# Kernel optimization log

Measured on AMD Instinct MI355X. Metric: run time of the kernel, lower is better.

Reference implementation:

```python
import jax, jax.numpy as jnp
import numpy as np

K = 9            # connections per output pixel
GA = 2           # global additional samples
RA = 2           # relative additional samples
VS = 4 + GA + RA # 2^rank neighbours + sampled
REGION = 12      # int(0.25 * 48) per spatial dim
MMULT = 0.1
MIN_SIGMA = 0.05
SIGMA_SCALE = 0.05
SIGMA_BOOST = 2.0


def setup_inputs() -> dict:
    key = jax.random.key(0)
    ks = jax.random.split(key, 8)
    b, cin, h, w = 8, 128, 48, 48
    cout = 256
    hidden = cin * 4

    def lin_init(k, fan_out, fan_in):
        bound = 1.0 / np.sqrt(fan_in)
        kw, kb = jax.random.split(k)
        W = jax.random.uniform(kw, (fan_out, fan_in), minval=-bound, maxval=bound, dtype=jnp.float32)
        bb = jax.random.uniform(kb, (fan_out,), minval=-bound, maxval=bound, dtype=jnp.float32)
        return W, bb

    x = jax.random.normal(ks[0], (b, cin, h, w), dtype=jnp.float32)
    W1, b1 = lin_init(ks[1], hidden, 2)          # toparams layer 1 (adaptive=False -> 2 coord inputs)
    W2, b2 = lin_init(ks[2], 3 * K, hidden)      # toparams layer 2 -> k means (2d) + k sigmas
    Wu, bu = lin_init(ks[3], cout, K * cin)      # unify linear
    gints = jax.random.randint(ks[4], (b, h, w, K, GA, 2), 0, h, dtype=jnp.int32)      # global samples (h==w)
    roff = jax.random.randint(ks[5], (b, h, w, K, RA, 2), 0, REGION, dtype=jnp.int32)  # relative offsets
    return {"x": x, "W1": W1, "b1": b1, "W2": W2, "b2": b2, "Wu": Wu, "bu": bu,
            "gints": gints, "roff": roff}


def reference(x, W1, b1, W2, b2, Wu, bu, gints, roff):
    b, c, h, w = x.shape
    s = jnp.array([h, w], dtype=x.dtype)                       # spatial range per dim
    s_int = jnp.array([h, w], dtype=jnp.int32)

    # normalized coordinate grid in [0,1], (h, w, 2) with [.,.,0]=row, [.,.,1]=col
    rows = jnp.arange(h, dtype=x.dtype) / (h - 1)
    cols = jnp.arange(w, dtype=x.dtype) / (w - 1)
    coords = jnp.stack(jnp.meshgrid(rows, cols, indexing='ij'), axis=-1)

    # hypernetwork: per-pixel coords -> K 2d mean offsets + K sigmas
    inp = jnp.broadcast_to(coords, (b, h, w, 2))
    hid = jax.nn.relu(inp @ W1.T + b1)
    params = hid @ W2.T + b2                                   # (b,h,w,3K)
    means_raw = params[..., :2 * K].reshape(b, h, w, K, 2)
    sig_raw = params[..., 2 * K:]                              # (b,h,w,K)

    # mids: inverse of the sigmoid scaling applied to the pixel's own coordinate
    pix = coords * (s - 1)                                     # pixel coordinates
    sc = pix / (s - 1) * 0.9999 + 0.00005
    mids = jnp.log(sc / (1.0 - sc))                            # (h,w,2)

    # transform_means: sigmoid -> [0, s-1]
    means = jax.nn.sigmoid(mids[None, :, :, None, :] + MMULT * means_raw) * (s - 1)  # (b,h,w,K,2)
    # transform_sigmas: softplus(. + boost) + min, per-dim scale, then sigma_scale
    sigmas = (jax.nn.softplus(sig_raw + SIGMA_BOOST) + MIN_SIGMA)[..., None] * s * SIGMA_SCALE  # (b,h,w,K,2)

    # ---- integer index generation (non-differentiable) ----
    fl = jnp.floor(jax.lax.stop_gradient(means)).astype(jnp.int32)   # (b,h,w,K,2)
    combos = jnp.array([[0, 0], [0, 1], [1, 0], [1, 1]], dtype=jnp.int32)
    neigh = fl[..., None, :] + combos                                 # (b,h,w,K,4,2)
    rel = fl[..., None, :] + roff - REGION // 2                       # (b,h,w,K,RA,2)
    ints = jnp.concatenate([neigh, gints, rel], axis=-2) % s_int      # (b,h,w,K,VS,2)

    # duplicate masking: zero any tuple that occurred earlier along VS
    eq = jnp.all(ints[..., :, None, :] == ints[..., None, :, :], axis=-1)  # (...,VS,VS)
    lower = jnp.tril(jnp.ones((VS, VS), dtype=bool), k=-1)
    dups = jnp.any(eq & lower, axis=-1)                               # (b,h,w,K,VS)

    # unnormalized gaussian densities of integer points under (means, sigmas)
    diff = (ints.astype(x.dtype) - means[..., None, :]) / sigmas[..., None, :]
    props = jnp.exp(-0.5 * jnp.sum(diff * diff, axis=-1))             # (b,h,w,K,VS)
    props = jnp.where(dups, jnp.zeros((), x.dtype), props)
    weights = props / jnp.sum(props, axis=-1, keepdims=True)          # mvalues are all-ones

    # irregular gather of input channel vectors at sampled pixels
    lin = ints[..., 0] * w + ints[..., 1]                             # (b,h,w,K,VS)
    flat = x.transpose(0, 2, 3, 1).reshape(b, h * w, c)
    feats = flat[jnp.arange(b)[:, None], lin.reshape(b, -1)]          # (b, h*w*K*VS, c)
    feats = feats.reshape(b, h, w, K, VS, c)

    feats = jnp.einsum('bhwkvc,bhwkv->bhwkc', feats, weights)         # weighted reduce over VS
    feats = feats.reshape(b, h, w, K * c)
    out = feats @ Wu.T + bu                                           # unify linear
    return out.transpose(0, 3, 1, 2)                                  # (b, cout, h, w)
```

## Files before the change

kernel.cpp:

```cpp
#include <hip/hip_runtime.h>
#include <hip/hip_bf16.h>
#include <hip/hip_fp16.h>

#define BB 8
#define CIN 128
#define HH 48
#define WW 48
#define HW 2304
#define KK 9
#define COUT 256
#define KC 1152
#define MM 18432
#define MT 32
#define SFP 136
#define NP 5

#define LIGHT_BARRIER() asm volatile("s_waitcnt lgkmcnt(0)\n\ts_barrier" ::: "memory")

typedef short bf16x8_t __attribute__((ext_vector_type(8)));
typedef float f32x16_t __attribute__((ext_vector_type(16)));
typedef float f32x4_t  __attribute__((ext_vector_type(4)));

static __device__ __forceinline__ float b2f(short u) {
    union { unsigned int i; float f; } c;
    c.i = ((unsigned int)(unsigned short)u) << 16;
    return c.f;
}

__global__ __launch_bounds__(256) void prep_kernel(
    const float* __restrict__ x, __hip_bfloat16* __restrict__ xT,
    const float* __restrict__ Wu, bf16x8_t* __restrict__ Bp,
    const float* __restrict__ W1, const float* __restrict__ b1,
    const float* __restrict__ W2, const float* __restrict__ b2,
    float* __restrict__ means, float* __restrict__ sigmas, int* __restrict__ fls)
{
    int bid = blockIdx.x;
    int t = threadIdx.x;

    if (bid < 576) {
        __shared__ float tile[64][65];
        int ij0 = (bid % 36) * 64;
        int c0  = ((bid / 36) % 2) * 64;
        int b   = bid / 72;
        int ijl = t & 63, cl = t >> 6;
        #pragma unroll
        for (int i = 0; i < 16; i++) {
            int cc = i*4 + cl;
            tile[cc][ijl] = x[(size_t)(b*CIN + c0 + cc) * HW + ij0 + ijl];
        }
        __syncthreads();
        int cl2 = t & 63, ijl2 = t >> 6;
        #pragma unroll
        for (int i = 0; i < 16; i++) {
            int ij = i*4 + ijl2;
            xT[(size_t)(b*HW + ij0 + ij) * CIN + c0 + cl2] = __float2bfloat16(tile[cl2][ij]);
        }
    } else if (bid < 720) {
        int idx = (bid - 576) * 256 + t;
        int lane = idx & 63;
        int rest = idx >> 6;
        int s = rest % 72, g = rest / 72;
        int r = lane & 31, qq = lane >> 5;
        const float* src = Wu + (size_t)(g*32 + r) * KC + s*16 + qq*8;
        union { bf16x8_t v; __hip_bfloat16 h[8]; } o;
        #pragma unroll
        for (int j = 0; j < 8; j++) o.h[j] = __float2bfloat16(src[j]);
        Bp[idx] = o.v;
    } else {
        int wave = t >> 6, lane = t & 63;
        int p = (bid - 720) * 4 + wave;
        int iy = p / WW, ix = p % WW;
        float ryf = (float)iy / 47.0f;
        float rxf = (float)ix / 47.0f;
        double ry = (double)ryf, rx = (double)rxf;

        double h[8];
        #pragma unroll
        for (int jj = 0; jj < 8; jj++) {
            int j = lane*8 + jj;
            double v = ry * (double)W1[j*2+0] + rx * (double)W1[j*2+1] + (double)b1[j];
            h[jj] = v > 0.0 ? v : 0.0;
        }
        double par[27];
        #pragma unroll
        for (int o = 0; o < 27; o++) {
            const float4* w4 = (const float4*)(W2 + (size_t)o*512 + lane*8);
            float4 wa = w4[0], wb = w4[1];
            double s = (double)wa.x*h[0] + (double)wa.y*h[1]
                     + (double)wa.z*h[2] + (double)wa.w*h[3]
                     + (double)wb.x*h[4] + (double)wb.y*h[5]
                     + (double)wb.z*h[6] + (double)wb.w*h[7];
            par[o] = s;
        }
        #pragma unroll
        for (int o = 0; o < 27; o++) {
            #pragma unroll
            for (int d = 1; d < 64; d <<= 1)
                par[o] += __shfl_xor(par[o], d, 64);
            par[o] += (double)b2[o];
        }
        if (lane < KK) {
            int k = lane;
            double scy = ry * 0.9999 + 5e-05;
            double scx = rx * 0.9999 + 5e-05;
            double midy = log(scy / (1.0 - scy));
            double midx = log(scx / (1.0 - scx));
            double zy = midy + 0.1 * par[2*k+0];
            double zx = midx + 0.1 * par[2*k+1];
            double my = 47.0 / (1.0 + exp(-zy));
            double mx = 47.0 / (1.0 + exp(-zx));
            double sr = par[18 + k] + 2.0;
            double sp = (sr > 0.0 ? sr : 0.0) + log1p(exp(-fabs(sr)));
            double sg = (sp + 0.05) * 48.0 * 0.05;
            means[(p*KK + k)*2 + 0] = (float)my;
            means[(p*KK + k)*2 + 1] = (float)mx;
            sigmas[p*KK + k] = (float)sg;
            fls[(p*KK + k)*2 + 0] = (int)floor(my);
            fls[(p*KK + k)*2 + 1] = (int)floor(mx);
        }
    }
}

__global__ __launch_bounds__(512, 4) void fused_kernel(
    const float* __restrict__ means, const float* __restrict__ sigmas,
    const int* __restrict__ fls, const int* __restrict__ gints,
    const int* __restrict__ roff, const short* __restrict__ xT,
    const bf16x8_t* __restrict__ Bp, const float* __restrict__ bu,
    float* __restrict__ out)
{
    __shared__ unsigned int s_tap[KK*MT*8];
    __shared__ __align__(16) short s_feat[2][2][MT*SFP];

    int t = threadIdx.x;
    int b   = blockIdx.x & 7;
    int grp = blockIdx.x >> 3;
    int ij0 = grp * MT;
    int m0  = b * HW + ij0;

    if (t < KK*MT) {
        int p = t;
        int k = p >> 5, row = p & 31;
        int ij = ij0 + row;
        int bij = m0 + row;
        int fy = fls[(ij*KK + k)*2 + 0];
        int fx = fls[(ij*KK + k)*2 + 1];
        float my = means[(ij*KK + k)*2 + 0];
        float mx = means[(ij*KK + k)*2 + 1];
        float sg = sigmas[ij*KK + k];
        int lins[8]; float ws[8];
        #pragma unroll
        for (int v = 0; v < 8; v++) {
            int iy, ix;
            if (v < 4) {
                iy = fy + (v >> 1); ix = fx + (v & 1);
            } else if (v < 6) {
                int base = ((bij*KK + k)*2 + (v - 4)) * 2;
                iy = gints[base]; ix = gints[base + 1];
            } else {
                int base = ((bij*KK + k)*2 + (v - 6)) * 2;
                iy = fy + roff[base] - 6; ix = fx + roff[base + 1] - 6;
            }
            iy = ((iy % HH) + HH) % HH;
            ix = ((ix % WW) + WW) % WW;
            lins[v] = iy * WW + ix;
            float dy = ((float)iy - my) / sg;
            float dx = ((float)ix - mx) / sg;
            ws[v] = expf(-0.5f * (dy*dy + dx*dx));
        }
        #pragma unroll
        for (int v = 1; v < 8; v++) {
            bool dup = false;
            #pragma unroll
            for (int u = 0; u < 8; u++) if (u < v) dup = dup || (lins[u] == lins[v]);
            if (dup) ws[v] = 0.0f;
        }
        float sum = 0.0f;
        #pragma unroll
        for (int v = 0; v < 8; v++) sum += ws[v];
        float inv = 1.0f / sum;
        #pragma unroll
        for (int v = 0; v < 8; v++) {
            unsigned short hb = __half_as_ushort(__float2half(ws[v] * inv));
            s_tap[p*8+v] = ((unsigned int)lins[v] << 16) | (unsigned int)hb;
        }
    }
    LIGHT_BARRIER();

    const short* xb = xT + (size_t)b * (HW * CIN);
    int lane = t & 63, wave = t >> 6;
    int r = lane & 31, q = lane >> 5;
    int cpart = t >> 8;
    int grow = (t >> 3) & 31;
    int gc0 = (t & 7) << 4;

    f32x16_t acc = {};

    for (int p = 0; p < NP; p++) {
        int kg = 2*p + cpart;
        if (kg < KK) {
            const unsigned int* tp = &s_tap[(kg*MT + grow)*8];
            unsigned int e[8];
            #pragma unroll
            for (int v = 0; v < 8; v++) e[v] = tp[v];
            bf16x8_t d0[8], d1[8];
            #pragma unroll
            for (int v = 0; v < 8; v++) {
                const bf16x8_t* sp = (const bf16x8_t*)(xb + (size_t)(e[v] >> 16) * CIN + gc0);
                d0[v] = sp[0];
                d1[v] = sp[1];
            }
            float a0[16];
            #pragma unroll
            for (int j = 0; j < 16; j++) a0[j] = 0.0f;
            #pragma unroll
            for (int v = 0; v < 8; v++) {
                float w = __half2float(__ushort_as_half((unsigned short)(e[v] & 0xffffu)));
                #pragma unroll
                for (int j = 0; j < 8; j++) {
                    a0[j]   += w * b2f(d0[v][j]);
                    a0[8+j] += w * b2f(d1[v][j]);
                }
            }
            union { bf16x8_t v8; __hip_bfloat16 hh[8]; } o0, o1;
            #pragma unroll
            for (int j = 0; j < 8; j++) {
                o0.hh[j] = __float2bfloat16(a0[j]);
                o1.hh[j] = __float2bfloat16(a0[8+j]);
            }
            bf16x8_t* fd = (bf16x8_t*)(&s_feat[p & 1][cpart][grow*SFP + gc0]);
            fd[0] = o0.v8;
            fd[1] = o1.v8;
        }
        LIGHT_BARRIER();
        #pragma unroll
        for (int cc = 0; cc < 2; cc++) {
            int k = 2*p + cc;
            if (k < KK) {
                const short* fb = s_feat[p & 1][cc];
                int base = (wave*72 + k*8)*64 + lane;
                #pragma unroll
                for (int si = 0; si < 8; si++) {
                    bf16x8_t Bf = Bp[base + si*64];
                    bf16x8_t a = *(const bf16x8_t*)(fb + r*SFP + si*16 + q*8);
                    acc = __builtin_amdgcn_mfma_f32_32x32x16_bf16(a, Bf, acc, 0, 0, 0);
                }
            }
        }
    }

    int n = wave*32 + r;
    float bv = bu[n];
    float* oc = out + ((size_t)b * COUT + n) * HW + ij0;
    #pragma unroll
    for (int g4 = 0; g4 < 4; g4++) {
        f32x4_t vv;
        vv[0] = acc[g4*4+0] + bv;
        vv[1] = acc[g4*4+1] + bv;
        vv[2] = acc[g4*4+2] + bv;
        vv[3] = acc[g4*4+3] + bv;
        *(f32x4_t*)(oc + g4*8 + q*4) = vv;
    }
}

extern "C" void kernel_launch(void* const* d_in, const int* in_sizes, int n_in,
                              void* d_out, int out_size, void* d_ws, size_t ws_size,
                              hipStream_t stream)
{
    const float* x   = (const float*)d_in[0];
    const float* W1  = (const float*)d_in[1];
    const float* b1  = (const float*)d_in[2];
    const float* W2  = (const float*)d_in[3];
    const float* b2  = (const float*)d_in[4];
    const float* Wu  = (const float*)d_in[5];
    const float* bu  = (const float*)d_in[6];
    const int* gints = (const int*)d_in[7];
    const int* roff  = (const int*)d_in[8];
    float* out = (float*)d_out;

    char* ws = (char*)d_ws;
    float* ws_means  = (float*)(ws + 0);
    float* ws_sigma  = (float*)(ws + 165888);
    int*   ws_fl     = (int*  )(ws + 248832);
    short* ws_xT     = (short*)(ws + 414720);
    bf16x8_t* ws_bp  = (bf16x8_t*)(ws + 5133312);

    prep_kernel<<<1296, 256, 0, stream>>>(x, (__hip_bfloat16*)ws_xT, Wu, ws_bp,
                                          W1, b1, W2, b2,
                                          ws_means, ws_sigma, ws_fl);
    fused_kernel<<<MM/MT, 512, 0, stream>>>(ws_means, ws_sigma, ws_fl, gints, roff,
                                            ws_xT, ws_bp, bu, out);
}
```

Baseline: 150.1 us.

## Split tap/weight computation into a separate kernel writing packed taps to global

Moves the per-pixel sample index and Gaussian weight computation out of the fused gather-GEMM kernel into its own fully parallel kernel. That kernel writes packed index/weight words to a global workspace. The fused kernel then loads them as 16-byte vectors instead of computing them with only 288 of 512 threads and waiting at a barrier. This removes the serial prologue and frees LDS. In exchange it adds a kernel launch and a global round trip of about 5.3 MB of tap data.

```diff
diff --git a/kernel.cpp b/kernel.cpp
--- a/kernel.cpp
+++ b/kernel.cpp
@@ -20,6 +20,7 @@
 typedef short bf16x8_t __attribute__((ext_vector_type(8)));
 typedef float f32x16_t __attribute__((ext_vector_type(16)));
 typedef float f32x4_t  __attribute__((ext_vector_type(4)));
+typedef unsigned int uint4_t __attribute__((ext_vector_type(4)));
 
 static __device__ __forceinline__ float b2f(short u) {
     union { unsigned int i; float f; } c;
@@ -121,70 +122,77 @@
     }
 }
 
-__global__ __launch_bounds__(512, 4) void fused_kernel(
+__global__ __launch_bounds__(256) void taps_kernel(
     const float* __restrict__ means, const float* __restrict__ sigmas,
     const int* __restrict__ fls, const int* __restrict__ gints,
-    const int* __restrict__ roff, const short* __restrict__ xT,
+    const int* __restrict__ roff, unsigned int* __restrict__ Tg)
+{
+    int idx = blockIdx.x * 256 + threadIdx.x;
+    int bij = idx / KK;
+    int k   = idx - bij * KK;
+    int ij  = bij % HW;
+
+    int fy = fls[(ij*KK + k)*2 + 0];
+    int fx = fls[(ij*KK + k)*2 + 1];
+    float my = means[(ij*KK + k)*2 + 0];
+    float mx = means[(ij*KK + k)*2 + 1];
+    float sg = sigmas[ij*KK + k];
+
+    int lins[8]; float ws[8];
+    #pragma unroll
+    for (int v = 0; v < 8; v++) {
+        int iy, ix;
+        if (v < 4) {
+            iy = fy + (v >> 1); ix = fx + (v & 1);
+        } else if (v < 6) {
+            int base = ((bij*KK + k)*2 + (v - 4)) * 2;
+            iy = gints[base]; ix = gints[base + 1];
+        } else {
+            int base = ((bij*KK + k)*2 + (v - 6)) * 2;
+            iy = fy + roff[base] - 6; ix = fx + roff[base + 1] - 6;
+        }
+        iy = ((iy % HH) + HH) % HH;
+        ix = ((ix % WW) + WW) % WW;
+        lins[v] = iy * WW + ix;
+        float dy = ((float)iy - my) / sg;
+        float dx = ((float)ix - mx) / sg;
+        ws[v] = expf(-0.5f * (dy*dy + dx*dx));
+    }
+    #pragma unroll
+    for (int v = 1; v < 8; v++) {
+        bool dup = false;
+        #pragma unroll
+        for (int u = 0; u < 8; u++) if (u < v) dup = dup || (lins[u] == lins[v]);
+        if (dup) ws[v] = 0.0f;
+    }
+    float sum = 0.0f;
+    #pragma unroll
+    for (int v = 0; v < 8; v++) sum += ws[v];
+    float inv = 1.0f / sum;
+    uint4_t o0, o1;
+    #pragma unroll
+    for (int v = 0; v < 4; v++) {
+        unsigned short hb = __half_as_ushort(__float2half(ws[v] * inv));
+        o0[v] = ((unsigned int)lins[v] << 16) | (unsigned int)hb;
+        unsigned short hb2 = __half_as_ushort(__float2half(ws[4+v] * inv));
+        o1[v] = ((unsigned int)lins[4+v] << 16) | (unsigned int)hb2;
+    }
+    uint4_t* dst = (uint4_t*)(Tg + (size_t)bij*72 + k*8);
+    dst[0] = o0;
+    dst[1] = o1;
+}
+
+__global__ __launch_bounds__(512, 4) void fused_kernel(
+    const unsigned int* __restrict__ Tg, const short* __restrict__ xT,
     const bf16x8_t* __restrict__ Bp, const float* __restrict__ bu,
     float* __restrict__ out)
 {
-    __shared__ unsigned int s_tap[KK*MT*8];
     __shared__ __align__(16) short s_feat[2][2][MT*SFP];
 
     int t = threadIdx.x;
     int b   = blockIdx.x & 7;
     int grp = blockIdx.x >> 3;
     int ij0 = grp * MT;
-    int m0  = b * HW + ij0;
-
-    if (t < KK*MT) {
-        int p = t;
-        int k = p >> 5, row = p & 31;
-        int ij = ij0 + row;
-        int bij = m0 + row;
-        int fy = fls[(ij*KK + k)*2 + 0];
-        int fx = fls[(ij*KK + k)*2 + 1];
-        float my = means[(ij*KK + k)*2 + 0];
-        float mx = means[(ij*KK + k)*2 + 1];
-        float sg = sigmas[ij*KK + k];
-        int lins[8]; float ws[8];
-        #pragma unroll
-        for (int v = 0; v < 8; v++) {
-            int iy, ix;
-            if (v < 4) {
-                iy = fy + (v >> 1); ix = fx + (v & 1);
-            } else if (v < 6) {
-                int base = ((bij*KK + k)*2 + (v - 4)) * 2;
-                iy = gints[base]; ix = gints[base + 1];
-            } else {
-                int base = ((bij*KK + k)*2 + (v - 6)) * 2;
-                iy = fy + roff[base] - 6; ix = fx + roff[base + 1] - 6;
-            }
-            iy = ((iy % HH) + HH) % HH;
-            ix = ((ix % WW) + WW) % WW;
-            lins[v] = iy * WW + ix;
-            float dy = ((float)iy - my) / sg;
-            float dx = ((float)ix - mx) / sg;
-            ws[v] = expf(-0.5f * (dy*dy + dx*dx));
-        }
-        #pragma unroll
-        for (int v = 1; v < 8; v++) {
-            bool dup = false;
-            #pragma unroll
-            for (int u = 0; u < 8; u++) if (u < v) dup = dup || (lins[u] == lins[v]);
-            if (dup) ws[v] = 0.0f;
-        }
-        float sum = 0.0f;
-        #pragma unroll
-        for (int v = 0; v < 8; v++) sum += ws[v];
-        float inv = 1.0f / sum;
-        #pragma unroll
-        for (int v = 0; v < 8; v++) {
-            unsigned short hb = __half_as_ushort(__float2half(ws[v] * inv));
-            s_tap[p*8+v] = ((unsigned int)lins[v] << 16) | (unsigned int)hb;
-        }
-    }
-    LIGHT_BARRIER();
 
     const short* xb = xT + (size_t)b * (HW * CIN);
     int lane = t & 63, wave = t >> 6;
@@ -193,15 +201,17 @@
     int grow = (t >> 3) & 31;
     int gc0 = (t & 7) << 4;
 
+    const unsigned int* tb = Tg + ((size_t)(b*HW + ij0) + grow) * 72;
+
     f32x16_t acc = {};
 
     for (int p = 0; p < NP; p++) {
         int kg = 2*p + cpart;
         if (kg < KK) {
-            const unsigned int* tp = &s_tap[(kg*MT + grow)*8];
-            unsigned int e[8];
-            #pragma unroll
-            for (int v = 0; v < 8; v++) e[v] = tp[v];
+            const uint4_t* tp = (const uint4_t*)(tb + kg*8);
+            uint4_t e0 = tp[0], e1 = tp[1];
+            unsigned int e[8] = {e0[0], e0[1], e0[2], e0[3],
+                                 e1[0], e1[1], e1[2], e1[3]};
             bf16x8_t d0[8], d1[8];
             #pragma unroll
             for (int v = 0; v < 8; v++) {
@@ -283,10 +293,12 @@
     int*   ws_fl     = (int*  )(ws + 248832);
     short* ws_xT     = (short*)(ws + 414720);
     bf16x8_t* ws_bp  = (bf16x8_t*)(ws + 5133312);
+    unsigned int* ws_tg = (unsigned int*)(ws + 5723136);
 
     prep_kernel<<<1296, 256, 0, stream>>>(x, (__hip_bfloat16*)ws_xT, Wu, ws_bp,
                                           W1, b1, W2, b2,
                                           ws_means, ws_sigma, ws_fl);
-    fused_kernel<<<MM/MT, 512, 0, stream>>>(ws_means, ws_sigma, ws_fl, gints, roff,
-                                            ws_xT, ws_bp, bu, out);
-}
+    taps_kernel<<<648, 256, 0, stream>>>(ws_means, ws_sigma, ws_fl, gints, roff,
+                                         ws_tg);
+    fused_kernel<<<MM/MT, 512, 0, stream>>>(ws_tg, ws_xT, ws_bp, bu, out);
+}
```

Measured after the change: 150.8 us. No clear change (+0.5%).
